# Kernel optimization log

Hardware: AMD Instinct MI355X
Metric: run time of the kernel (lower is better)

Reference implementation:

```python
import jax, jax.numpy as jnp
import numpy as np

NUM_HEADS = 16

def setup_inputs() -> dict:
    key = jax.random.key(0)
    ks = jax.random.split(key, 7)
    B, S, D = 2, 2048, 1024
    X = jax.random.normal(ks[0], (B, S, D), dtype=jnp.float32)
    s = 1.0 / np.sqrt(D)
    Wq = jax.random.normal(ks[1], (D, D), dtype=jnp.float32) * s
    Wk = jax.random.normal(ks[2], (D, D), dtype=jnp.float32) * s
    Wv = jax.random.normal(ks[3], (D, D), dtype=jnp.float32) * s
    Wo = jax.random.normal(ks[4], (D, D), dtype=jnp.float32) * s
    bo = jnp.zeros((D,), dtype=jnp.float32)
    return {"X": X, "Wq": Wq, "Wk": Wk, "Wv": Wv, "Wo": Wo, "bo": bo}

def reference(X, Wq, Wk, Wv, Wo, bo):
    B, S, D = X.shape
    H = NUM_HEADS
    hd = D // H
    # project and split heads -> [B, H, S, hd]
    def split(t):
        return t.reshape(B, S, H, hd).transpose(0, 2, 1, 3)
    q = split(X @ Wq)
    k = split(X @ Wk)
    v = split(X @ Wv)
    scores = jnp.einsum('bhqd,bhkd->bhqk', q, k) / jnp.sqrt(jnp.float32(hd))
    causal = jnp.tril(jnp.ones((S, S), dtype=bool))
    scores = jnp.where(causal, scores, -jnp.inf)
    weights = jax.nn.softmax(scores, axis=-1)  # dropout p=0 -> identity
    ctx = jnp.einsum('bhqk,bhkd->bhqd', weights, v)
    ctx = ctx.transpose(0, 2, 1, 3).reshape(B, S, D)
    return ctx @ Wo + bo
```

## Files before the change

### kernel.cpp

```cpp
#include <hip/hip_runtime.h>


typedef __attribute__((ext_vector_type(8))) short short8;
typedef __attribute__((ext_vector_type(4))) float floatx4;

__device__ inline unsigned short f2bf(float f) {
  unsigned u = __float_as_uint(f);
  unsigned r = (u + 0x7fffu + ((u >> 16) & 1u)) >> 16;
  return (unsigned short)r;
}

__device__ __forceinline__ float fast_exp2(float x) {
#if __has_builtin(__builtin_amdgcn_exp2f)
  return __builtin_amdgcn_exp2f(x);
#else
  float r;
  asm volatile("v_exp_f32_e32 %0, %1" : "=v"(r) : "v"(x));
  return r;
#endif
}

__device__ __forceinline__ void gll16(const unsigned short* g, unsigned short* l) {
  __builtin_amdgcn_global_load_lds(
      (const __attribute__((address_space(1))) unsigned int*)(g),
      (__attribute__((address_space(3))) unsigned int*)(l),
      16, 0, 0);
}

constexpr int B_ = 2, S_ = 2048, D_ = 1024, H_ = 16, HD_ = 64;

__global__ __launch_bounds__(256) void prep_inputs(
    const float* __restrict__ x, unsigned short* __restrict__ xb,
    const float* __restrict__ w0, const float* __restrict__ w1,
    const float* __restrict__ w2, const float* __restrict__ w3,
    unsigned short* __restrict__ wt_base)
{
  if (blockIdx.z == 4) {
    const int tid = threadIdx.y * 32 + threadIdx.x;
    const size_t base =
        ((size_t)(blockIdx.y * 32 + blockIdx.x) * 256 + tid) * 16;
#pragma unroll
    for (int half = 0; half < 2; ++half) {
      const size_t i = base + half * 8;
      float4 a = *(const float4*)(x + i);
      float4 b = *(const float4*)(x + i + 4);
      short8 o;
      o[0] = (short)f2bf(a.x); o[1] = (short)f2bf(a.y);
      o[2] = (short)f2bf(a.z); o[3] = (short)f2bf(a.w);
      o[4] = (short)f2bf(b.x); o[5] = (short)f2bf(b.y);
      o[6] = (short)f2bf(b.z); o[7] = (short)f2bf(b.w);
      *(short8*)(xb + i) = o;
    }
    return;
  }
  const float* src;
  switch (blockIdx.z) {
    case 0: src = w0; break;
    case 1: src = w1; break;
    case 2: src = w2; break;
    default: src = w3; break;
  }
  unsigned short* dst = wt_base + (size_t)blockIdx.z * 1024 * 1024;
  __shared__ unsigned short t[32][33];
  const int bx = blockIdx.x * 32;
  const int by = blockIdx.y * 32;
  const int x_ = threadIdx.x;
  for (int yy = threadIdx.y; yy < 32; yy += 8)
    t[yy][x_] = f2bf(src[(size_t)(by + yy) * 1024 + bx + x_]);
  __syncthreads();
  for (int yy = threadIdx.y; yy < 32; yy += 8)
    dst[(size_t)(bx + yy) * 1024 + by + x_] = t[x_][yy];
}

__global__ __launch_bounds__(256) void transpose_v(
    const unsigned short* __restrict__ Vb, unsigned short* __restrict__ Vt)
{
  __shared__ unsigned short t[32][33];
  const int bh = blockIdx.z;
  const int b = bh >> 4, h = bh & 15;
  const int s0 = blockIdx.x * 32, d0 = blockIdx.y * 32;
  const int x = threadIdx.x;
  for (int yy = threadIdx.y; yy < 32; yy += 8)
    t[yy][x] = Vb[(size_t)(b * 2048 + s0 + yy) * 1024 + h * 64 + d0 + x];
  __syncthreads();
  for (int yy = threadIdx.y; yy < 32; yy += 8)
    Vt[((size_t)bh * 64 + d0 + yy) * 2048 + s0 + x] = t[x][yy];
}

__global__ __launch_bounds__(256) void gemm256_qkv(
    const unsigned short* __restrict__ A,
    const unsigned short* __restrict__ Bt,
    unsigned short* __restrict__ Qo,
    unsigned short* __restrict__ Ko,
    unsigned short* __restrict__ Vo)
{
  __shared__ unsigned short sA[2][128 * 32];
  __shared__ unsigned short sB[2][128 * 32];
  const int K = 1024;
  const int m0 = blockIdx.y * 128;
  const int bn0 = blockIdx.x * 128;

  const int tid = threadIdx.x, wave = tid >> 6, lane = tid & 63;
  const int g = lane >> 4, ml = lane & 15;
  const int wm = wave & 1, wn = wave >> 1;

  const unsigned short* ag0 = A + (size_t)(m0 + (tid >> 2)) * K + (tid & 3) * 8;
  const unsigned short* ag1 = ag0 + (size_t)64 * K;
  const unsigned short* bg0 = Bt + (size_t)(bn0 + (tid >> 2)) * K + (tid & 3) * 8;
  const unsigned short* bg1 = bg0 + (size_t)64 * K;
  const int woff = wave * 512;

  floatx4 acc[4][4];
#pragma unroll
  for (int mt = 0; mt < 4; ++mt)
#pragma unroll
    for (int nt = 0; nt < 4; ++nt) acc[mt][nt] = (floatx4){0.f, 0.f, 0.f, 0.f};

  for (int k0 = 0; k0 < K; k0 += 64) {
    __syncthreads();
#pragma unroll
    for (int t = 0; t < 2; ++t) {
      gll16(ag0 + k0 + t * 32, sA[t] + woff);
      gll16(ag1 + k0 + t * 32, sA[t] + 2048 + woff);
      gll16(bg0 + k0 + t * 32, sB[t] + woff);
      gll16(bg1 + k0 + t * 32, sB[t] + 2048 + woff);
    }
    __syncthreads();
#pragma unroll
    for (int t = 0; t < 2; ++t) {
      short8 af[4], bf[4];
#pragma unroll
      for (int mt = 0; mt < 4; ++mt)
        af[mt] = *(const short8*)(sA[t] + (wm * 64 + mt * 16 + ml) * 32 + g * 8);
#pragma unroll
      for (int nt = 0; nt < 4; ++nt)
        bf[nt] = *(const short8*)(sB[t] + (wn * 64 + nt * 16 + ml) * 32 + g * 8);
#pragma unroll
      for (int mt = 0; mt < 4; ++mt)
#pragma unroll
        for (int nt = 0; nt < 4; ++nt)
          acc[mt][nt] = __builtin_amdgcn_mfma_f32_16x16x32_bf16(
              af[mt], bf[nt], acc[mt][nt], 0, 0, 0);
    }
  }

  const int proj = blockIdx.x >> 3;
  unsigned short* out = (proj == 0) ? Qo : (proj == 1) ? Ko : Vo;
  const int col0 = (blockIdx.x & 7) * 128;
#pragma unroll
  for (int mt = 0; mt < 4; ++mt) {
#pragma unroll
    for (int nt = 0; nt < 4; ++nt) {
      const int col = col0 + wn * 64 + nt * 16 + ml;
#pragma unroll
      for (int r = 0; r < 4; ++r) {
        const int row = m0 + wm * 64 + mt * 16 + g * 4 + r;
        out[(size_t)row * 1024 + col] = f2bf(acc[mt][nt][r]);
      }
    }
  }
}

__global__ __launch_bounds__(256) void gemm_wo64(
    const unsigned short* __restrict__ A,
    const unsigned short* __restrict__ Bt,
    const float* __restrict__ bias,
    float* __restrict__ C)
{
  __shared__ unsigned short sA[4][64 * 32];
  __shared__ unsigned short sB[4][128 * 32];
  const int K = 1024;
  const int m0 = blockIdx.y * 64;
  const int bn0 = blockIdx.x * 128;
  const int tid = threadIdx.x, wave = tid >> 6, lane = tid & 63;
  const int g = lane >> 4, ml = lane & 15;
  const int wm = wave & 1, wn = wave >> 1;

  const unsigned short* ag =
      A + (size_t)(m0 + wave * 16 + (lane >> 2)) * K + (lane & 3) * 8;
  const unsigned short* bg0 = Bt + (size_t)(bn0 + (tid >> 2)) * K + (tid & 3) * 8;
  const unsigned short* bg1 = bg0 + (size_t)64 * K;
  const int woff = wave * 512;

  floatx4 acc[2][4];
#pragma unroll
  for (int mt = 0; mt < 2; ++mt)
#pragma unroll
    for (int nt = 0; nt < 4; ++nt) acc[mt][nt] = (floatx4){0.f, 0.f, 0.f, 0.f};

  for (int k0 = 0; k0 < K; k0 += 128) {
    __syncthreads();
#pragma unroll
    for (int t = 0; t < 4; ++t) {
      gll16(ag + k0 + t * 32, sA[t] + woff);
      gll16(bg0 + k0 + t * 32, sB[t] + woff);
      gll16(bg1 + k0 + t * 32, sB[t] + 2048 + woff);
    }
    __syncthreads();
#pragma unroll
    for (int t = 0; t < 4; ++t) {
      short8 af[2], bf[4];
#pragma unroll
      for (int mt = 0; mt < 2; ++mt)
        af[mt] = *(const short8*)(sA[t] + (wm * 32 + mt * 16 + ml) * 32 + g * 8);
#pragma unroll
      for (int nt = 0; nt < 4; ++nt)
        bf[nt] = *(const short8*)(sB[t] + (wn * 64 + nt * 16 + ml) * 32 + g * 8);
#pragma unroll
      for (int mt = 0; mt < 2; ++mt)
#pragma unroll
        for (int nt = 0; nt < 4; ++nt)
          acc[mt][nt] = __builtin_amdgcn_mfma_f32_16x16x32_bf16(
              af[mt], bf[nt], acc[mt][nt], 0, 0, 0);
    }
  }

#pragma unroll
  for (int mt = 0; mt < 2; ++mt) {
#pragma unroll
    for (int nt = 0; nt < 4; ++nt) {
      const int col = bn0 + wn * 64 + nt * 16 + ml;
      const float badd = bias[col];
#pragma unroll
      for (int r = 0; r < 4; ++r) {
        const int row = m0 + wm * 32 + mt * 16 + g * 4 + r;
        C[(size_t)row * 1024 + col] = acc[mt][nt][r] + badd;
      }
    }
  }
}

constexpr int LDP = 72;
constexpr int KTPB = 2;

struct AttnLds {
  unsigned short k0[KTPB][64 * 32];
  unsigned short k1[KTPB][64 * 32];
  unsigned short v0[KTPB][64 * 32];
  unsigned short v1[KTPB][64 * 32];
  unsigned short p[8 * 16 * LDP];
};
union __align__(16) AttnLdsU {
  AttnLds t;
  float comb[4 * 64 * 40];
};

__device__ __forceinline__ void attn_tile(
    const short8* aq,
    const unsigned short* sK0, const unsigned short* sK1,
    const unsigned short* sV0, const unsigned short* sV1,
    unsigned short* pw, floatx4* acc, float* l,
    const bool diag, const int qrow0, const int kcol0,
    const int g, const int ml)
{
  const float C1 = 0.18033688f;
  const float C2 = -34.6246810f;

  floatx4 s[4];
#pragma unroll
  for (int nb = 0; nb < 4; ++nb) {
    s[nb] = (floatx4){0.f, 0.f, 0.f, 0.f};
    short8 bk0 = *(const short8*)(sK0 + (nb * 16 + ml) * 32 + g * 8);
    s[nb] = __builtin_amdgcn_mfma_f32_16x16x32_bf16(aq[0], bk0, s[nb], 0, 0, 0);
    short8 bk1 = *(const short8*)(sK1 + (nb * 16 + ml) * 32 + g * 8);
    s[nb] = __builtin_amdgcn_mfma_f32_16x16x32_bf16(aq[1], bk1, s[nb], 0, 0, 0);
  }
#pragma unroll
  for (int r = 0; r < 4; ++r) {
    const int qrow = qrow0 + g * 4 + r;
    float rowsum = 0.f;
#pragma unroll
    for (int nb = 0; nb < 4; ++nb) {
      float wv = fast_exp2(fmaf(s[nb][r], C1, C2));
      if (diag && (kcol0 + nb * 16 + ml > qrow)) wv = 0.f;
      const unsigned bits = __float_as_uint(wv);
      pw[(g * 4 + r) * LDP + nb * 16 + ml] = (unsigned short)(bits >> 16);
      rowsum += __uint_as_float(bits & 0xffff0000u);
    }
    l[r] += rowsum;
  }
#pragma unroll
  for (int st = 0; st < 2; ++st) {
    short8 ap = *(const short8*)(pw + ml * LDP + st * 32 + g * 8);
    const unsigned short* sv = st ? sV1 : sV0;
#pragma unroll
    for (int jd = 0; jd < 4; ++jd) {
      short8 bv = *(const short8*)(sv + (jd * 16 + ml) * 32 + g * 8);
      acc[jd] = __builtin_amdgcn_mfma_f32_16x16x32_bf16(ap, bv, acc[jd], 0, 0, 0);
    }
  }
}

__global__ __launch_bounds__(512) void attn_v11(
    const unsigned short* __restrict__ Q,
    const unsigned short* __restrict__ Kg,
    const unsigned short* __restrict__ Vt,
    unsigned short* __restrict__ CTX)
{
  __shared__ AttnLdsU lds;

  const int bh = blockIdx.y;
  const int b = bh >> 4, h = bh & 15;
  const int p = blockIdx.x;
  const int qbA = p, qbB = 31 - p;
  const int qA0 = qbA * 64, qB0 = qbB * 64;
  const int tid = threadIdx.x, w = tid >> 6, lane = tid & 63;
  const int slice = w & 3, par = w >> 2;
  const int g = lane >> 4, ml = lane & 15;

  const size_t headoff = (size_t)b * S_ * D_ + (size_t)h * HD_;
  const size_t vtoff   = (size_t)bh * HD_ * S_;

  short8 aqA[2], aqB[2];
  {
    const unsigned short* qp =
        Q + headoff + (size_t)(qA0 + slice * 16 + ml) * D_ + g * 8;
    aqA[0] = *(const short8*)qp;
    aqA[1] = *(const short8*)(qp + 32);
  }
  {
    const unsigned short* qp =
        Q + headoff + (size_t)(qB0 + slice * 16 + ml) * D_ + g * 8;
    aqB[0] = *(const short8*)qp;
    aqB[1] = *(const short8*)(qp + 32);
  }

  floatx4 accA[4], accB[4];
#pragma unroll
  for (int jd = 0; jd < 4; ++jd) {
    accA[jd] = (floatx4){0.f, 0.f, 0.f, 0.f};
    accB[jd] = (floatx4){0.f, 0.f, 0.f, 0.f};
  }
  float lA[4] = {0.f, 0.f, 0.f, 0.f};
  float lB[4] = {0.f, 0.f, 0.f, 0.f};

  const int sw = slice;
  const unsigned short* kgb =
      Kg + headoff + (size_t)(sw * 16 + (lane >> 2)) * D_ + (lane & 3) * 8;
  const unsigned short* vgb =
      Vt + vtoff + (size_t)(sw * 16 + (lane >> 2)) * S_ + (lane & 3) * 8;
  unsigned short* pw = lds.t.p + w * 16 * LDP;
  const int woff = sw * 512;

  const int ntiles = qbB + 1;
  for (int kt0 = 0; kt0 < ntiles; kt0 += KTPB) {
    const int cnt = (ntiles - kt0 < KTPB) ? (ntiles - kt0) : KTPB;
    __syncthreads();
#pragma unroll
    for (int t = 0; t < KTPB; ++t) {
      if (t >= cnt) break;
      const int kt = kt0 + t;
      if (w < 4) {
        const size_t ko = (size_t)kt * 64 * D_;
        gll16(kgb + ko,      lds.t.k0[t] + woff);
        gll16(kgb + ko + 32, lds.t.k1[t] + woff);
      } else {
        gll16(vgb + kt * 64,      lds.t.v0[t] + woff);
        gll16(vgb + kt * 64 + 32, lds.t.v1[t] + woff);
      }
    }
    __syncthreads();

    if (par < cnt) {
      const int kt = kt0 + par;
      attn_tile(aqB, lds.t.k0[par], lds.t.k1[par], lds.t.v0[par], lds.t.v1[par],
                pw, accB, lB, kt == qbB, qB0 + slice * 16, kt * 64, g, ml);
      if (kt <= qbA)
        attn_tile(aqA, lds.t.k0[par], lds.t.k1[par], lds.t.v0[par], lds.t.v1[par],
                  pw, accA, lA, kt == qbA, qA0 + slice * 16, kt * 64, g, ml);
    }
  }

  __syncthreads();
  {
    float* slot = lds.comb + (size_t)(slice * 64 + lane) * 40;
    if (par == 1) {
#pragma unroll
      for (int jd = 0; jd < 4; ++jd) {
        *(floatx4*)(slot + jd * 4) = accA[jd];
        *(floatx4*)(slot + 20 + jd * 4) = accB[jd];
      }
#pragma unroll
      for (int r = 0; r < 4; ++r) {
        slot[16 + r] = lA[r];
        slot[36 + r] = lB[r];
      }
    }
    __syncthreads();
    if (par == 1) return;
#pragma unroll
    for (int jd = 0; jd < 4; ++jd) {
      accA[jd] += *(const floatx4*)(slot + jd * 4);
      accB[jd] += *(const floatx4*)(slot + 20 + jd * 4);
    }
#pragma unroll
    for (int r = 0; r < 4; ++r) {
      lA[r] += slot[16 + r];
      lB[r] += slot[36 + r];
    }
  }

#pragma unroll
  for (int r = 0; r < 4; ++r) {
    float la = lA[r];
    la += __shfl_xor(la, 1); la += __shfl_xor(la, 2);
    la += __shfl_xor(la, 4); la += __shfl_xor(la, 8);
    lA[r] = 1.0f / la;
    float lb = lB[r];
    lb += __shfl_xor(lb, 1); lb += __shfl_xor(lb, 2);
    lb += __shfl_xor(lb, 4); lb += __shfl_xor(lb, 8);
    lB[r] = 1.0f / lb;
  }
#pragma unroll
  for (int r = 0; r < 4; ++r) {
    const int rowA = qA0 + slice * 16 + g * 4 + r;
    const int rowB = qB0 + slice * 16 + g * 4 + r;
#pragma unroll
    for (int jd = 0; jd < 4; ++jd) {
      CTX[headoff + (size_t)rowA * D_ + jd * 16 + ml] = f2bf(accA[jd][r] * lA[r]);
      CTX[headoff + (size_t)rowB * D_ + jd * 16 + ml] = f2bf(accB[jd][r] * lB[r]);
    }
  }
}

extern "C" void kernel_launch(void* const* d_in, const int* in_sizes, int n_in,
                              void* d_out, int out_size, void* d_ws, size_t ws_size,
                              hipStream_t stream)
{
  const float* X  = (const float*)d_in[0];
  const float* Wq = (const float*)d_in[1];
  const float* Wk = (const float*)d_in[2];
  const float* Wv = (const float*)d_in[3];
  const float* Wo = (const float*)d_in[4];
  const float* bo = (const float*)d_in[5];

  char* ws = (char*)d_ws;
  const size_t MB = 1024 * 1024;

  unsigned short* Qb  = (unsigned short*)(ws);
  unsigned short* Kb  = (unsigned short*)(ws + 8 * MB);
  unsigned short* Xb  = (unsigned short*)(ws + 16 * MB);
  unsigned short* WT  = (unsigned short*)(ws + 24 * MB);
  unsigned short* WoT = WT + (size_t)3 * 1024 * 1024;
  unsigned short* Vb  = (unsigned short*)d_out;
  unsigned short* Vt  = Xb;

  prep_inputs<<<dim3(32, 32, 5), dim3(32, 8), 0, stream>>>(
      X, Xb, Wq, Wk, Wv, Wo, WT);
  gemm256_qkv<<<dim3(24, 32), 256, 0, stream>>>(Xb, WT, Qb, Kb, Vb);
  transpose_v<<<dim3(64, 2, 32), dim3(32, 8), 0, stream>>>(Vb, Vt);
  attn_v11<<<dim3(16, B_ * H_), 512, 0, stream>>>(Qb, Kb, Vt, Qb);
  gemm_wo64<<<dim3(8, 64), 256, 0, stream>>>(Qb, WoT, bo, (float*)d_out);
}
```

Before: 205.5 us.

## Keep attention probabilities in registers via transposed S and permlane swaps

The QK^T MFMA operands are swapped so each lane holds scores for a single query row across several keys. The bf16 probabilities are then packed with perm and redistributed with v_permlane32/16_swap into the A-operand layout for the PV MFMA. This removes the LDS round-trip (store plus reload) of the P tile and shrinks the row-sum bookkeeping to one scalar per lane. The cost is extra permute instructions and more register pressure, and correctness depends on the permlane mapping matching the MFMA operand layout.

```diff
diff --git a/kernel.cpp b/kernel.cpp
--- a/kernel.cpp
+++ b/kernel.cpp
@@ -230,7 +230,6 @@
   }
 }
 
-constexpr int LDP = 72;
 constexpr int KTPB = 2;
 
 struct AttnLds {
@@ -238,19 +237,18 @@
   unsigned short k1[KTPB][64 * 32];
   unsigned short v0[KTPB][64 * 32];
   unsigned short v1[KTPB][64 * 32];
-  unsigned short p[8 * 16 * LDP];
 };
 union __align__(16) AttnLdsU {
   AttnLds t;
-  float comb[4 * 64 * 40];
+  float comb[4 * 64 * 36];
 };
 
 __device__ __forceinline__ void attn_tile(
     const short8* aq,
     const unsigned short* sK0, const unsigned short* sK1,
     const unsigned short* sV0, const unsigned short* sV1,
-    unsigned short* pw, floatx4* acc, float* l,
-    const bool diag, const int qrow0, const int kcol0,
+    floatx4* acc, float& l,
+    const bool diag, const int qg , const int kb ,
     const int g, const int ml)
 {
   const float C1 = 0.18033688f;
@@ -261,28 +259,51 @@
   for (int nb = 0; nb < 4; ++nb) {
     s[nb] = (floatx4){0.f, 0.f, 0.f, 0.f};
     short8 bk0 = *(const short8*)(sK0 + (nb * 16 + ml) * 32 + g * 8);
-    s[nb] = __builtin_amdgcn_mfma_f32_16x16x32_bf16(aq[0], bk0, s[nb], 0, 0, 0);
+    s[nb] = __builtin_amdgcn_mfma_f32_16x16x32_bf16(bk0, aq[0], s[nb], 0, 0, 0);
     short8 bk1 = *(const short8*)(sK1 + (nb * 16 + ml) * 32 + g * 8);
-    s[nb] = __builtin_amdgcn_mfma_f32_16x16x32_bf16(aq[1], bk1, s[nb], 0, 0, 0);
-  }
-#pragma unroll
-  for (int r = 0; r < 4; ++r) {
-    const int qrow = qrow0 + g * 4 + r;
-    float rowsum = 0.f;
-#pragma unroll
-    for (int nb = 0; nb < 4; ++nb) {
+    s[nb] = __builtin_amdgcn_mfma_f32_16x16x32_bf16(bk1, aq[1], s[nb], 0, 0, 0);
+  }
+
+  unsigned wb[4][4];
+#pragma unroll
+  for (int nb = 0; nb < 4; ++nb) {
+#pragma unroll
+    for (int r = 0; r < 4; ++r) {
       float wv = fast_exp2(fmaf(s[nb][r], C1, C2));
-      if (diag && (kcol0 + nb * 16 + ml > qrow)) wv = 0.f;
-      const unsigned bits = __float_as_uint(wv);
-      pw[(g * 4 + r) * LDP + nb * 16 + ml] = (unsigned short)(bits >> 16);
-      rowsum += __uint_as_float(bits & 0xffff0000u);
-    }
-    l[r] += rowsum;
-  }
-#pragma unroll
-  for (int st = 0; st < 2; ++st) {
-    short8 ap = *(const short8*)(pw + ml * LDP + st * 32 + g * 8);
-    const unsigned short* sv = st ? sV1 : sV0;
+      if (diag && (kb + nb * 16 + r > qg)) wv = 0.f;
+      const unsigned bits = __float_as_uint(wv) & 0xffff0000u;
+      wb[nb][r] = bits;
+      l += __uint_as_float(bits);
+    }
+  }
+
+  unsigned pk[4][2];
+#pragma unroll
+  for (int nb = 0; nb < 4; ++nb) {
+    pk[nb][0] = __builtin_amdgcn_perm(wb[nb][1], wb[nb][0], 0x07060302u);
+    pk[nb][1] = __builtin_amdgcn_perm(wb[nb][3], wb[nb][2], 0x07060302u);
+  }
+
+  unsigned Fr[2][4];
+#pragma unroll
+  for (int rr = 0; rr < 2; ++rr) {
+    unsigned a0 = pk[0][rr], a1 = pk[1][rr];
+    unsigned a2 = pk[2][rr], a3 = pk[3][rr];
+    asm("v_permlane32_swap_b32 %0, %1" : "+v"(a0), "+v"(a1));
+    asm("v_permlane32_swap_b32 %0, %1" : "+v"(a2), "+v"(a3));
+    asm("v_permlane16_swap_b32 %0, %1" : "+v"(a0), "+v"(a1));
+    asm("v_permlane16_swap_b32 %0, %1" : "+v"(a2), "+v"(a3));
+    Fr[0][rr] = a0; Fr[0][2 + rr] = a1;
+    Fr[1][rr] = a2; Fr[1][2 + rr] = a3;
+  }
+
+#pragma unroll
+  for (int f = 0; f < 2; ++f) {
+    union { unsigned u[4]; short8 s8; } uap;
+    uap.u[0] = Fr[f][0]; uap.u[1] = Fr[f][1];
+    uap.u[2] = Fr[f][2]; uap.u[3] = Fr[f][3];
+    const short8 ap = uap.s8;
+    const unsigned short* sv = f ? sV1 : sV0;
 #pragma unroll
     for (int jd = 0; jd < 4; ++jd) {
       short8 bv = *(const short8*)(sv + (jd * 16 + ml) * 32 + g * 8);
@@ -291,7 +312,7 @@
   }
 }
 
-__global__ __launch_bounds__(512) void attn_v11(
+__global__ __launch_bounds__(512) void attn_v12(
     const unsigned short* __restrict__ Q,
     const unsigned short* __restrict__ Kg,
     const unsigned short* __restrict__ Vt,
@@ -331,15 +352,15 @@
     accA[jd] = (floatx4){0.f, 0.f, 0.f, 0.f};
     accB[jd] = (floatx4){0.f, 0.f, 0.f, 0.f};
   }
-  float lA[4] = {0.f, 0.f, 0.f, 0.f};
-  float lB[4] = {0.f, 0.f, 0.f, 0.f};
+  float lA = 0.f, lB = 0.f;
+  const int qgA = qA0 + slice * 16 + ml;
+  const int qgB = qB0 + slice * 16 + ml;
 
   const int sw = slice;
   const unsigned short* kgb =
       Kg + headoff + (size_t)(sw * 16 + (lane >> 2)) * D_ + (lane & 3) * 8;
   const unsigned short* vgb =
       Vt + vtoff + (size_t)(sw * 16 + (lane >> 2)) * S_ + (lane & 3) * 8;
-  unsigned short* pw = lds.t.p + w * 16 * LDP;
   const int woff = sw * 512;
 
   const int ntiles = qbB + 1;
@@ -363,62 +384,57 @@
 
     if (par < cnt) {
       const int kt = kt0 + par;
+      const int kb = kt * 64 + g * 4;
       attn_tile(aqB, lds.t.k0[par], lds.t.k1[par], lds.t.v0[par], lds.t.v1[par],
-                pw, accB, lB, kt == qbB, qB0 + slice * 16, kt * 64, g, ml);
+                accB, lB, kt == qbB, qgB, kb, g, ml);
       if (kt <= qbA)
         attn_tile(aqA, lds.t.k0[par], lds.t.k1[par], lds.t.v0[par], lds.t.v1[par],
-                  pw, accA, lA, kt == qbA, qA0 + slice * 16, kt * 64, g, ml);
+                  accA, lA, kt == qbA, qgA, kb, g, ml);
     }
   }
 
   __syncthreads();
   {
-    float* slot = lds.comb + (size_t)(slice * 64 + lane) * 40;
+    float* slot = lds.comb + (size_t)(slice * 64 + lane) * 36;
     if (par == 1) {
 #pragma unroll
       for (int jd = 0; jd < 4; ++jd) {
         *(floatx4*)(slot + jd * 4) = accA[jd];
-        *(floatx4*)(slot + 20 + jd * 4) = accB[jd];
+        *(floatx4*)(slot + 16 + jd * 4) = accB[jd];
       }
-#pragma unroll
-      for (int r = 0; r < 4; ++r) {
-        slot[16 + r] = lA[r];
-        slot[36 + r] = lB[r];
-      }
+      slot[32] = lA;
+      slot[33] = lB;
     }
     __syncthreads();
     if (par == 1) return;
 #pragma unroll
     for (int jd = 0; jd < 4; ++jd) {
       accA[jd] += *(const floatx4*)(slot + jd * 4);
-      accB[jd] += *(const floatx4*)(slot + 20 + jd * 4);
-    }
-#pragma unroll
-    for (int r = 0; r < 4; ++r) {
-      lA[r] += slot[16 + r];
-      lB[r] += slot[36 + r];
-    }
-  }
-
+      accB[jd] += *(const floatx4*)(slot + 16 + jd * 4);
+    }
+    lA += slot[32];
+    lB += slot[33];
+  }
+
+  lA += __shfl_xor(lA, 16); lA += __shfl_xor(lA, 32);
+  lB += __shfl_xor(lB, 16); lB += __shfl_xor(lB, 32);
+  const float liA = 1.0f / lA;
+  const float liB = 1.0f / lB;
+  float lrA[4], lrB[4];
 #pragma unroll
   for (int r = 0; r < 4; ++r) {
-    float la = lA[r];
-    la += __shfl_xor(la, 1); la += __shfl_xor(la, 2);
-    la += __shfl_xor(la, 4); la += __shfl_xor(la, 8);
-    lA[r] = 1.0f / la;
-    float lb = lB[r];
-    lb += __shfl_xor(lb, 1); lb += __shfl_xor(lb, 2);
-    lb += __shfl_xor(lb, 4); lb += __shfl_xor(lb, 8);
-    lB[r] = 1.0f / lb;
-  }
+    lrA[r] = __shfl(liA, g * 4 + r);
+    lrB[r] = __shfl(liB, g * 4 + r);
+  }
+
 #pragma unroll
   for (int r = 0; r < 4; ++r) {
     const int rowA = qA0 + slice * 16 + g * 4 + r;
     const int rowB = qB0 + slice * 16 + g * 4 + r;
 #pragma unroll
     for (int jd = 0; jd < 4; ++jd) {
-      CTX[headoff + (size_t)rowA * D_ + jd * 16 + ml] = f2bf(accA[jd][r] * lA[r]);
-      CTX[headoff + (size_t)rowB * D_ + jd * 16 + ml] = f2bf(accB[jd][r] * lB[r]);
+      CTX[headoff + (size_t)rowA * D_ + jd * 16 + ml] = f2bf(accA[jd][r] * lrA[r]);
+      CTX[headoff + (size_t)rowB * D_ + jd * 16 + ml] = f2bf(accB[jd][r] * lrB[r]);
     }
   }
 }
@@ -449,6 +465,6 @@
       X, Xb, Wq, Wk, Wv, Wo, WT);
   gemm256_qkv<<<dim3(24, 32), 256, 0, stream>>>(Xb, WT, Qb, Kb, Vb);
   transpose_v<<<dim3(64, 2, 32), dim3(32, 8), 0, stream>>>(Vb, Vt);
-  attn_v11<<<dim3(16, B_ * H_), 512, 0, stream>>>(Qb, Kb, Vt, Qb);
+  attn_v12<<<dim3(16, B_ * H_), 512, 0, stream>>>(Qb, Kb, Vt, Qb);
   gemm_wo64<<<dim3(8, 64), 256, 0, stream>>>(Qb, WoT, bo, (float*)d_out);
 }
```

Result: faster. 201.1 us (-2.2%).
